# Kernel optimization log

Measured on AMD Instinct MI355X. Metric: run time of the kernel, lower is better.

Reference implementation:

```python
import jax, jax.numpy as jnp
import numpy as np

D_HIST = 64
LO, HI = -3.0, 3.0
FALL_OFF = 0.02
EPS = 1e-6


def setup_inputs() -> dict:
    key = jax.random.key(0)
    k1, k2 = jax.random.split(key)
    x = jax.random.uniform(k1, (8, 3, 256, 256), dtype=jnp.float32)
    y = jax.random.uniform(k2, (8, 3, 256, 256), dtype=jnp.float32)
    return {"x": x, "y": y}


def _hist_feature(img):
    # img: (B, 3, H, W)
    B = img.shape[0]
    flat = (img + EPS).reshape(B, 3, -1)            # (B, 3, N)
    i_y = jnp.sqrt(jnp.sum(jnp.square(flat), axis=1))  # (B, N) pixel intensity
    lr, lg, lb = jnp.log(flat[:, 0]), jnp.log(flat[:, 1]), jnp.log(flat[:, 2])
    ur = lr - lg
    vr = lr - lb
    ug, vg = -ur, -ur + vr
    ub, vb = -vr, -vr + ur
    centers = jnp.linspace(LO, HI, D_HIST, dtype=img.dtype)  # (D,)

    def rbf(d):
        # inverse-quadratic kernel vs bin centers -> (B, N, D)
        return 1.0 / (1.0 + jnp.square(jnp.abs(d[..., None] - centers) / FALL_OFF))

    def hist_c(uc, vc):
        # weighted outer-product reduction over pixels (the bmm): (B, D, D)
        return jnp.einsum('bn,bnu,bnv->buv', i_y, rbf(uc), rbf(vc))

    hist = jnp.stack([hist_c(ur, vr), hist_c(ug, vg), hist_c(ub, vb)], axis=1)  # (B,3,D,D)
    total = jnp.sum(hist, axis=(1, 2, 3), keepdims=True)
    return hist / total


def reference(x, y):
    x_hist = _hist_feature(x)
    y_hist = _hist_feature(y)
    diff = jnp.sqrt(y_hist) - jnp.sqrt(x_hist)
    h = jnp.sum(jnp.square(diff), axis=(1, 2, 3))  # (B,)
    h_norm = jnp.sqrt(h) * jnp.sqrt(jnp.asarray(0.5, dtype=h.dtype))
    return jnp.mean(h_norm)
```

## Files before the change

### kernel.cpp

```cpp
#include <hip/hip_runtime.h>
#include <math.h>

#define N_PIX 65536
#define EPSF 1e-6f
#define CHUNKS 16
#define PX_PER_CHUNK 4096
#define PX_PER_WAVE 1024
#define N_TILES (PX_PER_WAVE / 64)
#define N_JOBS 48
#define N_BLOCKS (N_JOBS * CHUNKS)
#define LN2_50 34.65735903f

typedef __attribute__((ext_vector_type(2))) float f2;
using short8 = __attribute__((ext_vector_type(8))) short;
using f32x4  = __attribute__((ext_vector_type(4))) float;

__device__ __forceinline__ float rcp_fast(float x) { return __builtin_amdgcn_rcpf(x); }

#if __has_builtin(__builtin_amdgcn_cvt_pk_bf16_f32)
typedef __attribute__((ext_vector_type(2))) __bf16 bf16x2_t;
__device__ __forceinline__ uint32_t pk_bf16(float a, float b) {
    return __builtin_bit_cast(uint32_t, __builtin_amdgcn_cvt_pk_bf16_f32(a, b));
}
#else
__device__ __forceinline__ uint32_t pk_bf16(float a, float b) {
    const uint32_t ua = __builtin_bit_cast(uint32_t, a) + 0x8000u;
    const uint32_t ub = __builtin_bit_cast(uint32_t, b) + 0x8000u;
    return __builtin_amdgcn_perm(ub, ua, 0x07060302u);
}
#endif

__device__ __forceinline__ float4 phaseA(float pr, float pg, float pb, int c) {
    const float r  = pr + EPSF;
    const float g  = pg + EPSF;
    const float bl = pb + EPSF;
    const float wgt = sqrtf(fmaf(r, r, fmaf(g, g, bl * bl)));
    const float lr = __log2f(r), lg = __log2f(g), lb2 = __log2f(bl);
    const float l0 = (c == 0) ? lr : ((c == 1) ? lg : lb2);
    const float lu = (c == 0) ? lg : lr;
    const float lv = (c == 2) ? lg : lb2;
    return make_float4((l0 - lu) * LN2_50, (l0 - lv) * LN2_50, wgt, 0.0f);
}

__global__ __launch_bounds__(256, 4) void hist_kernel(
    const float* __restrict__ x, const float* __restrict__ y,
    float* __restrict__ partial, float* __restrict__ accum)
{
    const int blk = blockIdx.x;
    const int chunk = blk & (CHUNKS - 1);
    const int job = blk / CHUNKS;
    const int c = job % 3;
    const int ib = job / 3;
    const int img = ib >> 3;
    const int b = ib & 7;
    const float* __restrict__ src = (img == 0 ? x : y) + (size_t)b * 3 * N_PIX;

    const int tid = threadIdx.x;
    if (blk == 0 && tid < 24) accum[tid] = 0.0f;

    __shared__ __align__(16) float lds[4096];
    const int lane = tid & 63;
    const int wv = tid >> 6;
    float* __restrict__ wbuf = lds + wv * 288;

    const int quad = lane >> 4;
    const int l15 = lane & 15;
    f2 ncb01, ncb23;
    {
        const float c0 = (-3.0f + (float)(l15)      * (6.0f / 63.0f)) * 50.0f;
        const float c1 = (-3.0f + (float)(16 + l15) * (6.0f / 63.0f)) * 50.0f;
        const float c2 = (-3.0f + (float)(32 + l15) * (6.0f / 63.0f)) * 50.0f;
        const float c3 = (-3.0f + (float)(48 + l15) * (6.0f / 63.0f)) * 50.0f;
        ncb01 = (f2){-c0, -c1};
        ncb23 = (f2){-c2, -c3};
    }
    const f2 one2 = {1.0f, 1.0f};

    f32x4 acc[16];
#pragma unroll
    for (int i = 0; i < 16; ++i) acc[i] = (f32x4){0.f, 0.f, 0.f, 0.f};

    const int px0 = chunk * PX_PER_CHUNK + wv * PX_PER_WAVE;

    float pr, pg, pb;
    {
        const int n = px0 + lane;
        pr = src[n]; pg = src[N_PIX + n]; pb = src[2 * N_PIX + n];
    }

#pragma unroll 1
    for (int st = 0; st < N_TILES; ++st) {
        const float4 uvw = phaseA(pr, pg, pb, c);
        *(float4*)(wbuf + lane * 4 + (lane >> 3) * 4) = uvw;

        if (st + 1 < N_TILES) {
            const int n2 = px0 + (st + 1) * 64 + lane;
            pr = src[n2]; pg = src[N_PIX + n2]; pb = src[2 * N_PIX + n2];
        }

#pragma unroll
        for (int h = 0; h < 2; ++h) {
            const int base = h * 32 + quad * 8;
            const float4* __restrict__ pbase =
                (const float4*)(wbuf + base * 4 + (base >> 3) * 4);
            int aU[4][4], aV[4][4];

#pragma unroll
            for (int jp = 0; jp < 4; ++jp) {
                const float4 pe = pbase[2 * jp];
                const float4 po = pbase[2 * jp + 1];

                float aue[4], auo[4], bve[4], bvo[4];
#pragma unroll
                for (int eo = 0; eo < 2; ++eo) {
                    const float ru = eo ? po.x : pe.x;
                    const float rv = eo ? po.y : pe.y;
                    const float rw = eo ? po.z : pe.z;
                    float* au = eo ? auo : aue;
                    float* bv = eo ? bvo : bve;

                    const f2 ruu = {ru, ru};
                    const f2 tu01 = ruu + ncb01;
                    const f2 tu23 = ruu + ncb23;
                    const f2 qu01 = __builtin_elementwise_fma(tu01, tu01, one2);
                    const f2 qu23 = __builtin_elementwise_fma(tu23, tu23, one2);
                    const float pu01 = qu01.x * qu01.y;
                    const float pu23 = qu23.x * qu23.y;
                    const float Ru = rcp_fast(pu01 * pu23) * rw;
                    const float ru01 = Ru * pu23, ru23 = Ru * pu01;
                    au[0] = ru01 * qu01.y; au[1] = ru01 * qu01.x;
                    au[2] = ru23 * qu23.y; au[3] = ru23 * qu23.x;

                    const f2 rvv = {rv, rv};
                    const f2 tv01 = rvv + ncb01;
                    const f2 tv23 = rvv + ncb23;
                    const f2 qv01 = __builtin_elementwise_fma(tv01, tv01, one2);
                    const f2 qv23 = __builtin_elementwise_fma(tv23, tv23, one2);
                    const float pv01 = qv01.x * qv01.y;
                    const float pv23 = qv23.x * qv23.y;
                    const float Rv = rcp_fast(pv01 * pv23);
                    const float rv01 = Rv * pv23, rv23 = Rv * pv01;
                    bv[0] = rv01 * qv01.y; bv[1] = rv01 * qv01.x;
                    bv[2] = rv23 * qv23.y; bv[3] = rv23 * qv23.x;
                }
#pragma unroll
                for (int mt = 0; mt < 4; ++mt) {
                    aU[mt][jp] = pk_bf16(aue[mt], auo[mt]);
                    aV[mt][jp] = pk_bf16(bve[mt], bvo[mt]);
                }
            }

            short8 af[4], bf[4];
#pragma unroll
            for (int mt = 0; mt < 4; ++mt) {
                af[mt] = __builtin_bit_cast(short8,
                    make_int4(aU[mt][0], aU[mt][1], aU[mt][2], aU[mt][3]));
                bf[mt] = __builtin_bit_cast(short8,
                    make_int4(aV[mt][0], aV[mt][1], aV[mt][2], aV[mt][3]));
            }
#pragma unroll
            for (int mt = 0; mt < 4; ++mt)
#pragma unroll
                for (int nt = 0; nt < 4; ++nt)
                    acc[mt * 4 + nt] = __builtin_amdgcn_mfma_f32_16x16x32_bf16(
                        af[mt], bf[nt], acc[mt * 4 + nt], 0, 0, 0);
        }
    }

    float* __restrict__ outp = partial + (size_t)blk * 4096;
#pragma unroll 1
    for (int ch = 0; ch < 4; ++ch) {
        __syncthreads();
#pragma unroll
        for (int nt = 0; nt < 4; ++nt)
            *(f32x4*)(lds + wv * 1024 + nt * 256 + lane * 4) = acc[ch * 4 + nt];
        __syncthreads();
        const int e4 = tid * 4;
        const f32x4 s0 = *(const f32x4*)(lds +        e4);
        const f32x4 s1 = *(const f32x4*)(lds + 1024 + e4);
        const f32x4 s2 = *(const f32x4*)(lds + 2048 + e4);
        const f32x4 s3 = *(const f32x4*)(lds + 3072 + e4);
        const f32x4 s = (s0 + s1) + (s2 + s3);
        const int l = tid & 63;
        const int n = ((tid >> 6) << 4) | (l & 15);
        float* op = outp + (ch * 16 + (l >> 4) * 4) * 64 + n;
        op[0] = s.x; op[64] = s.y; op[128] = s.z; op[192] = s.w;
    }
}

__global__ __launch_bounds__(256) void reduce_cross_kernel(
    const float* __restrict__ partial, float* __restrict__ accum)
{
    const int jx = blockIdx.x >> 4;
    const int bb = jx / 3;
    const int e = ((blockIdx.x & 15) << 8) | threadIdx.x;
    const float* px = partial + (size_t)jx * CHUNKS * 4096 + e;
    const float* py = partial + (size_t)(24 + jx) * CHUNKS * 4096 + e;

    float sx = 0.0f, sy = 0.0f;
#pragma unroll
    for (int k = 0; k < CHUNKS; ++k) {
        sx += px[(size_t)k * 4096];
        sy += py[(size_t)k * 4096];
    }
    float cr = sqrtf(sx * sy);

#pragma unroll
    for (int o = 32; o > 0; o >>= 1) {
        sx += __shfl_down(sx, o, 64);
        sy += __shfl_down(sy, o, 64);
        cr += __shfl_down(cr, o, 64);
    }
    __shared__ float red[12];
    const int wv = threadIdx.x >> 6;
    if ((threadIdx.x & 63) == 0) {
        red[wv] = sx; red[4 + wv] = sy; red[8 + wv] = cr;
    }
    __syncthreads();
    if (threadIdx.x == 0) {
        atomicAdd(&accum[bb],      red[0] + red[1] + red[2] + red[3]);
        atomicAdd(&accum[8 + bb],  red[4] + red[5] + red[6] + red[7]);
        atomicAdd(&accum[16 + bb], red[8] + red[9] + red[10] + red[11]);
    }
}

__global__ void final_kernel(const float* __restrict__ accum, float* __restrict__ out)
{
    if (threadIdx.x == 0) {
        float s = 0.0f;
#pragma unroll
        for (int b = 0; b < 8; ++b) {
            const float rho = accum[16 + b] * __builtin_amdgcn_rsqf(accum[b] * accum[8 + b]);
            s += sqrtf(fmaxf(1.0f - rho, 0.0f));
        }
        out[0] = s * 0.125f;
    }
}

extern "C" void kernel_launch(void* const* d_in, const int* in_sizes, int n_in,
                              void* d_out, int out_size, void* d_ws, size_t ws_size,
                              hipStream_t stream)
{
    const float* x = (const float*)d_in[0];
    const float* y = (const float*)d_in[1];
    float* ws = (float*)d_ws;
    float* partial = ws;
    float* accum = ws + (size_t)N_BLOCKS * 4096;
    float* outf = (float*)d_out;

    hipLaunchKernelGGL(hist_kernel, dim3(N_BLOCKS), dim3(256), 0, stream,
                       x, y, partial, accum);
    hipLaunchKernelGGL(reduce_cross_kernel, dim3(24 * 16), dim3(256), 0, stream,
                       partial, accum);
    hipLaunchKernelGGL(final_kernel, dim3(1), dim3(64), 0, stream, accum, outf);
}
```

Before: 167.2 us.

## Fuse histogram, cross-reduction and final kernels with an atomic grid barrier

Merges the three launches into one kernel. Every block bumps a global counter when its partial histogram is written. The first 384 blocks then spin until all 768 have arrived, do the cross-image reduction, and the last finisher computes the final scalar. This removes two kernel launches and their gaps. In exchange it relies on all blocks being co-resident, and on block 0 zeroing the counters before any other block increments them, which is an ordering race.

```diff
diff --git a/kernel.cpp b/kernel.cpp
--- a/kernel.cpp
+++ b/kernel.cpp
@@ -42,10 +42,14 @@
     return make_float4((l0 - lu) * LN2_50, (l0 - lv) * LN2_50, wgt, 0.0f);
 }
 
-__global__ __launch_bounds__(256, 4) void hist_kernel(
+__global__ __launch_bounds__(256, 4) void fused_kernel(
     const float* __restrict__ x, const float* __restrict__ y,
-    float* __restrict__ partial, float* __restrict__ accum)
+    float* __restrict__ ws, float* __restrict__ out)
 {
+    float* __restrict__ partial = ws;
+    float* __restrict__ accum   = ws + (size_t)N_BLOCKS * 4096;
+    unsigned* __restrict__ ctr  = (unsigned*)(accum + 24);
+
     const int blk = blockIdx.x;
     const int chunk = blk & (CHUNKS - 1);
     const int job = blk / CHUNKS;
@@ -56,7 +60,7 @@
     const float* __restrict__ src = (img == 0 ? x : y) + (size_t)b * 3 * N_PIX;
 
     const int tid = threadIdx.x;
-    if (blk == 0 && tid < 24) accum[tid] = 0.0f;
+    if (blk == 0 && tid < 26) ((unsigned*)accum)[tid] = 0u;
 
     __shared__ __align__(16) float lds[4096];
     const int lane = tid & 63;
@@ -186,54 +190,72 @@
         float* op = outp + (ch * 16 + (l >> 4) * 4) * 64 + n;
         op[0] = s.x; op[64] = s.y; op[128] = s.z; op[192] = s.w;
     }
-}
-
-__global__ __launch_bounds__(256) void reduce_cross_kernel(
-    const float* __restrict__ partial, float* __restrict__ accum)
-{
-    const int jx = blockIdx.x >> 4;
-    const int bb = jx / 3;
-    const int e = ((blockIdx.x & 15) << 8) | threadIdx.x;
-    const float* px = partial + (size_t)jx * CHUNKS * 4096 + e;
-    const float* py = partial + (size_t)(24 + jx) * CHUNKS * 4096 + e;
-
-    float sx = 0.0f, sy = 0.0f;
-#pragma unroll
-    for (int k = 0; k < CHUNKS; ++k) {
-        sx += px[(size_t)k * 4096];
-        sy += py[(size_t)k * 4096];
-    }
-    float cr = sqrtf(sx * sy);
-
-#pragma unroll
-    for (int o = 32; o > 0; o >>= 1) {
-        sx += __shfl_down(sx, o, 64);
-        sy += __shfl_down(sy, o, 64);
-        cr += __shfl_down(cr, o, 64);
-    }
-    __shared__ float red[12];
-    const int wv = threadIdx.x >> 6;
-    if ((threadIdx.x & 63) == 0) {
-        red[wv] = sx; red[4 + wv] = sy; red[8 + wv] = cr;
-    }
+
     __syncthreads();
-    if (threadIdx.x == 0) {
-        atomicAdd(&accum[bb],      red[0] + red[1] + red[2] + red[3]);
-        atomicAdd(&accum[8 + bb],  red[4] + red[5] + red[6] + red[7]);
-        atomicAdd(&accum[16 + bb], red[8] + red[9] + red[10] + red[11]);
-    }
-}
-
-__global__ void final_kernel(const float* __restrict__ accum, float* __restrict__ out)
-{
-    if (threadIdx.x == 0) {
-        float s = 0.0f;
-#pragma unroll
-        for (int b = 0; b < 8; ++b) {
-            const float rho = accum[16 + b] * __builtin_amdgcn_rsqf(accum[b] * accum[8 + b]);
-            s += sqrtf(fmaxf(1.0f - rho, 0.0f));
-        }
-        out[0] = s * 0.125f;
+    if (tid == 0) {
+        __threadfence();
+        __hip_atomic_fetch_add(&ctr[0], 1u, __ATOMIC_RELEASE, __HIP_MEMORY_SCOPE_AGENT);
+    }
+    if (blk >= 24 * 16) return;
+
+    if (tid == 0) {
+        long spins = 0;
+        while (__hip_atomic_load(&ctr[0], __ATOMIC_ACQUIRE, __HIP_MEMORY_SCOPE_AGENT)
+                   < (unsigned)N_BLOCKS && spins < (1L << 30)) {
+            __builtin_amdgcn_s_sleep(8);
+            ++spins;
+        }
+    }
+    __syncthreads();
+
+    {
+        const int jx = blk >> 4;
+        const int bb = jx / 3;
+        const int e = ((blk & 15) << 8) | tid;
+        const float* px = partial + (size_t)jx * CHUNKS * 4096 + e;
+        const float* py = partial + (size_t)(24 + jx) * CHUNKS * 4096 + e;
+
+        float sx = 0.0f, sy = 0.0f;
+#pragma unroll
+        for (int k = 0; k < CHUNKS; ++k) {
+            sx += px[(size_t)k * 4096];
+            sy += py[(size_t)k * 4096];
+        }
+        float cr = sqrtf(sx * sy);
+
+#pragma unroll
+        for (int o = 32; o > 0; o >>= 1) {
+            sx += __shfl_down(sx, o, 64);
+            sy += __shfl_down(sy, o, 64);
+            cr += __shfl_down(cr, o, 64);
+        }
+        if ((tid & 63) == 0) {
+            lds[wv] = sx; lds[4 + wv] = sy; lds[8 + wv] = cr;
+        }
+        __syncthreads();
+        if (tid == 0) {
+            atomicAdd(&accum[bb],      lds[0] + lds[1] + lds[2] + lds[3]);
+            atomicAdd(&accum[8 + bb],  lds[4] + lds[5] + lds[6] + lds[7]);
+            atomicAdd(&accum[16 + bb], lds[8] + lds[9] + lds[10] + lds[11]);
+        }
+    }
+
+    if (tid == 0) {
+        __threadfence();
+        const unsigned old = __hip_atomic_fetch_add(&ctr[1], 1u,
+                                 __ATOMIC_ACQ_REL, __HIP_MEMORY_SCOPE_AGENT);
+        if (old == 24 * 16 - 1) {
+            float s = 0.0f;
+#pragma unroll
+            for (int bb = 0; bb < 8; ++bb) {
+                const float tx = __hip_atomic_load(&accum[bb],      __ATOMIC_ACQUIRE, __HIP_MEMORY_SCOPE_AGENT);
+                const float ty = __hip_atomic_load(&accum[8 + bb],  __ATOMIC_ACQUIRE, __HIP_MEMORY_SCOPE_AGENT);
+                const float cc = __hip_atomic_load(&accum[16 + bb], __ATOMIC_ACQUIRE, __HIP_MEMORY_SCOPE_AGENT);
+                const float rho = cc * __builtin_amdgcn_rsqf(tx * ty);
+                s += sqrtf(fmaxf(1.0f - rho, 0.0f));
+            }
+            out[0] = s * 0.125f;
+        }
     }
 }
 
@@ -244,13 +266,8 @@
     const float* x = (const float*)d_in[0];
     const float* y = (const float*)d_in[1];
     float* ws = (float*)d_ws;
-    float* partial = ws;
-    float* accum = ws + (size_t)N_BLOCKS * 4096;
     float* outf = (float*)d_out;
 
-    hipLaunchKernelGGL(hist_kernel, dim3(N_BLOCKS), dim3(256), 0, stream,
-                       x, y, partial, accum);
-    hipLaunchKernelGGL(reduce_cross_kernel, dim3(24 * 16), dim3(256), 0, stream,
-                       partial, accum);
-    hipLaunchKernelGGL(final_kernel, dim3(1), dim3(64), 0, stream, accum, outf);
-}
+    hipLaunchKernelGGL(fused_kernel, dim3(N_BLOCKS), dim3(256), 0, stream,
+                       x, y, ws, outf);
+}
```

Result: slower. 278.3 us (+66.4%).
